# Kernel optimization log

Hardware: AMD Instinct MI355X
Metric: run time of the kernel (lower is better)

## Reference

```python
import jax, jax.numpy as jnp
import numpy as np

POOLED_H = 7
POOLED_W = 7
SPATIAL_SCALE = 0.0625
B, C, H, W = 8, 256, 48, 48
R = 300
IMG = 768  # = H / SPATIAL_SCALE


def setup_inputs() -> dict:
    key = jax.random.key(0)
    k1, k2, k3, k4 = jax.random.split(key, 4)
    features = jax.random.normal(k1, (B, C, H, W), dtype=jnp.float32)
    # rois: (batch_idx, x1, y1, x2, y2) in input-image coords
    bidx = jax.random.randint(k2, (R, 1), 0, B).astype(jnp.float32)
    tl = jax.random.uniform(k3, (R, 2), minval=0.0, maxval=IMG - 64.0)
    wh = jax.random.uniform(k4, (R, 2), minval=32.0, maxval=320.0)
    br = jnp.minimum(tl + wh, IMG - 1.0)
    rois = jnp.concatenate([bidx, tl, br], axis=1).astype(jnp.float32)
    return {"features": features, "rois": rois}


def _hat_integral(x, grid):
    """Integral from -inf to x of the unit hat basis function centered at each
    grid point g (support [g-1, g+1], peak 1, total mass 1).
    x: [..., 1-broadcastable], grid: [G] -> returns [..., G]."""
    t = x[..., None] - (grid - 1.0)
    return jnp.where(
        t <= 0.0, 0.0,
        jnp.where(t <= 1.0, 0.5 * t * t,
                  jnp.where(t <= 2.0, 1.0 - 0.5 * (2.0 - t) ** 2, 1.0)))


def reference(features, rois):
    # Precise RoI Pooling: exact double integral of the bilinear interpolant
    # over each bin, divided by bin area. Bilinear interp (with zero padding
    # outside the map, as in the CUDA PrRoIPoolingGetData) is
    #   f(u,v) = sum_{j,i} feat[j,i] * hat_j(v) * hat_i(u)
    # so the bin integral factorizes into per-axis hat-integral weights.
    Bf, Cf, Hf, Wf = features.shape
    bidx = rois[:, 0].astype(jnp.int32)
    x1 = rois[:, 1] * SPATIAL_SCALE
    y1 = rois[:, 2] * SPATIAL_SCALE
    x2 = rois[:, 3] * SPATIAL_SCALE
    y2 = rois[:, 4] * SPATIAL_SCALE
    roi_w = jnp.maximum(x2 - x1, 0.0)
    roi_h = jnp.maximum(y2 - y1, 0.0)
    bin_w = roi_w / POOLED_W  # [R]
    bin_h = roi_h / POOLED_H

    ph = jnp.arange(POOLED_H, dtype=jnp.float32)
    pw = jnp.arange(POOLED_W, dtype=jnp.float32)
    ya = y1[:, None] + ph[None, :] * bin_h[:, None]  # [R, PH]
    yb = ya + bin_h[:, None]
    xa = x1[:, None] + pw[None, :] * bin_w[:, None]  # [R, PW]
    xb = xa + bin_w[:, None]

    gy = jnp.arange(Hf, dtype=jnp.float32)
    gx = jnp.arange(Wf, dtype=jnp.float32)
    Wy = _hat_integral(yb, gy) - _hat_integral(ya, gy)  # [R, PH, H]
    Wx = _hat_integral(xb, gx) - _hat_integral(xa, gx)  # [R, PW, W]

    feat = features[bidx]  # [R, C, H, W]
    t = jnp.einsum('rpj,rcji->rcpi', Wy, feat)   # integrate over y
    num = jnp.einsum('rqi,rcpi->rcpq', Wx, t)    # integrate over x -> [R,C,PH,PW]

    area = (bin_w * bin_h)[:, None, None, None]  # win_size per ROI
    out = jnp.where(area > 0.0, num / jnp.where(area > 0.0, area, 1.0), 0.0)
    return out
```

## Files before the change

### kernel.cpp

```cpp
#include <hip/hip_runtime.h>


#define PH 7
#define PW 7
#define NBINS 49
#define SCALE 0.0625f
#define CH 256
#define FH 48
#define FW 48
#define RNUM 300
#define CB 8
#define MAXJ 23
#define NL 7

__device__ __forceinline__ float hat_int(float x, float g) {
    float t = x - (g - 1.0f);
    if (t <= 0.0f) return 0.0f;
    if (t <= 1.0f) return 0.5f * t * t;
    if (t <= 2.0f) { float u = 2.0f - t; return 1.0f - 0.5f * u * u; }
    return 1.0f;
}

__global__ __launch_bounds__(256)
void prroi_fused(const float* __restrict__ feat,
                 const float* __restrict__ rois,
                 float* __restrict__ out) {
    const int cblk = blockIdx.x;
    const int r    = blockIdx.y;
    const int c0   = cblk * CB;
    const int tid  = threadIdx.x;

    __shared__ float patch[MAXJ * NL * 32];
    __shared__ float rs[PW * MAXJ * CB];
    __shared__ float pbuf[99];

    const float* roi = rois + r * 5;
    const int   b  = (int)roi[0];
    const float x1 = roi[1] * SCALE, y1 = roi[2] * SCALE;
    const float x2 = roi[3] * SCALE, y2 = roi[4] * SCALE;
    const float ylo = fminf(y1, y2), yhi = fmaxf(y1, y2);
    const float xlo = fminf(x1, x2), xhi = fmaxf(x1, x2);
    const int j1 = min(FH - 1, (int)floorf(yhi) + 1);
    const int i1 = min(FW - 1, (int)floorf(xhi) + 1);
    const int J0 = min(max(0, (int)floorf(ylo) - 1), FH - 6);
    const int I0 = min(max(0, (int)floorf(xlo) - 1) & ~3, FW - 8);
    const int JROWS = min(FH - J0, max(j1 - J0 + 1, 6));
    int NI4 = min(((i1 - I0) >> 2) + 1, (FW - I0) >> 2);
    NI4 = max(NI4, 2);

    const float roi_w = fmaxf(x2 - x1, 0.0f);
    const float bin_w = roi_w / (float)PW;
    const int nA = JROWS * 14;
    int pw1 = 0, q1 = 0, j1r = 0, pw2 = 0, q2 = 0, j2r = 0, bi1 = 0, bi2 = 0;
    float wxa[6], wxb[6];
    const bool a1 = tid < nA, a2 = (tid + 256) < nA;
    if (a1) {
        j1r = tid / 14; const int rem = tid - j1r * 14; pw1 = rem >> 1; q1 = rem & 1;
        const float xa = x1 + pw1 * bin_w, xb = xa + bin_w;
        const int base = min(max((int)floorf(xa) - 1, I0), I0 + 4 * NI4 - 6);
        bi1 = base - I0;
#pragma unroll
        for (int k = 0; k < 6; ++k) {
            const float g = (float)(base + k);
            wxa[k] = hat_int(xb, g) - hat_int(xa, g);
        }
    }
    if (a2) {
        const int v2 = tid + 256;
        j2r = v2 / 14; const int rem = v2 - j2r * 14; pw2 = rem >> 1; q2 = rem & 1;
        const float xa = x1 + pw2 * bin_w, xb = xa + bin_w;
        const int base = min(max((int)floorf(xa) - 1, I0), I0 + 4 * NI4 - 6);
        bi2 = base - I0;
#pragma unroll
        for (int k = 0; k < 6; ++k) {
            const float g = (float)(base + k);
            wxb[k] = hat_int(xb, g) - hat_int(xa, g);
        }
    }

    const float* fb = feat + (size_t)(b * CH + c0) * FH * FW;
    const int J7 = JROWS * NL;
    for (int u = tid; u < 2 * J7; u += 256) {
        const int q  = (u >= J7) ? 1 : 0;
        const int rm = u - q * J7;
        const int j  = rm / NL;
        const int i4 = rm - j * NL;
        if (i4 < NI4) {
            const int ig = I0 + 4 * i4;
            const float* src = fb + ((size_t)(4 * q) * FH + (J0 + j)) * FW + ig;
            const float4 v0  = *(const float4*)(src);
            const float4 v1v = *(const float4*)(src + FH * FW);
            const float4 v2v = *(const float4*)(src + 2 * FH * FW);
            const float4 v3v = *(const float4*)(src + 3 * FH * FW);
            const int msk = (j + i4) & 7;
            float* dl = &patch[(j * NL + i4) * 32];
            *(float4*)(dl + (((0 | q) ^ msk) << 2)) = make_float4(v0.x, v1v.x, v2v.x, v3v.x);
            *(float4*)(dl + (((2 | q) ^ msk) << 2)) = make_float4(v0.y, v1v.y, v2v.y, v3v.y);
            *(float4*)(dl + (((4 | q) ^ msk) << 2)) = make_float4(v0.z, v1v.z, v2v.z, v3v.z);
            *(float4*)(dl + (((6 | q) ^ msk) << 2)) = make_float4(v0.w, v1v.w, v2v.w, v3v.w);
        }
    }

    const float roi_h = fmaxf(y2 - y1, 0.0f);
    const float bin_h = roi_h / (float)PH;
    if (tid < PH) {
        const int ph = tid;
        const float ya = y1 + ph * bin_h, yb = ya + bin_h;
        const int base = min(max((int)floorf(ya) - 1, J0), J0 + JROWS - 6);
        pbuf[84 + ph] = __int_as_float(base - J0);
#pragma unroll
        for (int k = 0; k < 6; ++k) {
            const float g = (float)(base + k);
            pbuf[ph * 6 + k] = hat_int(yb, g) - hat_int(ya, g);
        }
    } else if (tid == PH) {
        const float area = bin_w * bin_h;
        pbuf[98] = (area > 0.0f) ? (1.0f / area) : 0.0f;
    }
    __syncthreads();

    if (a1) {
        float ax = 0.0f, ay = 0.0f, az = 0.0f, aw = 0.0f;
#pragma unroll
        for (int ii = 0; ii < 6; ++ii) {
            const float w = wxa[ii];
            const int i  = bi1 + ii;
            const int i4 = i >> 2, il = i & 3;
            const int slot = ((il << 1) | q1) ^ ((j1r + i4) & 7);
            const float4 v = *(const float4*)(&patch[(j1r * NL + i4) * 32 + (slot << 2)]);
            ax += w * v.x; ay += w * v.y; az += w * v.z; aw += w * v.w;
        }
        *(float4*)(&rs[((size_t)pw1 * MAXJ + j1r) * CB + ((q1 ^ (j1r & 1)) << 2)]) =
            make_float4(ax, ay, az, aw);
    }
    if (a2) {
        float ax = 0.0f, ay = 0.0f, az = 0.0f, aw = 0.0f;
#pragma unroll
        for (int ii = 0; ii < 6; ++ii) {
            const float w = wxb[ii];
            const int i  = bi2 + ii;
            const int i4 = i >> 2, il = i & 3;
            const int slot = ((il << 1) | q2) ^ ((j2r + i4) & 7);
            const float4 v = *(const float4*)(&patch[(j2r * NL + i4) * 32 + (slot << 2)]);
            ax += w * v.x; ay += w * v.y; az += w * v.z; aw += w * v.w;
        }
        *(float4*)(&rs[((size_t)pw2 * MAXJ + j2r) * CB + ((q2 ^ (j2r & 1)) << 2)]) =
            make_float4(ax, ay, az, aw);
    }
    __syncthreads();

    const int bin = tid & 63;
    const int cp  = tid >> 6;
    if (bin < NBINS) {
        const int phv = bin / PW, pwv = bin - phv * PW;
        const int bj = __float_as_int(pbuf[84 + phv]);
        const float inv_area = pbuf[98];
        const int qh = cp >> 1, lo = (cp & 1) * 2;
        float ax = 0.0f, ay = 0.0f;
#pragma unroll
        for (int jj = 0; jj < 6; ++jj) {
            const int j = bj + jj;
            const float w = pbuf[phv * 6 + jj];
            const float2 v = *(const float2*)(
                &rs[((size_t)pwv * MAXJ + j) * CB + ((qh ^ (j & 1)) << 2) + lo]);
            ax += w * v.x; ay += w * v.y;
        }
        float* o = out + ((size_t)r * CH + c0 + 2 * cp) * NBINS + bin;
        o[0]     = ax * inv_area;
        o[NBINS] = ay * inv_area;
    }
}

extern "C" void kernel_launch(void* const* d_in, const int* in_sizes, int n_in,
                              void* d_out, int out_size, void* d_ws, size_t ws_size,
                              hipStream_t stream) {
    const float* feat = (const float*)d_in[0];
    const float* rois = (const float*)d_in[1];
    float* out = (float*)d_out;
    (void)d_ws; (void)ws_size;

    prroi_fused<<<dim3(CH / CB, RNUM), 256, 0, stream>>>(feat, rois, out);
}
```

Baseline: 93.19 us.

## Convert to persistent kernel with register prefetch of next feature patch

Replaces the 9600-block grid with 768 persistent blocks, each handling a contiguous run of 12-13 (ROI, channel-block) work items. While the current item is being reduced from shared memory, the global loads for the next item's feature patch are issued into registers and written to shared memory afterwards. X and Y interpolation weights are recomputed only when the ROI changes. This targets per-block launch and setup cost and hides global-load latency behind compute. In exchange it adds register pressure from the prefetch buffers, an extra barrier when the ROI changes, and a fixed static split of work across blocks.

New measurement: 102.8 us. 1.1x slower.

```diff
diff --git a/kernel.cpp b/kernel.cpp
--- a/kernel.cpp
+++ b/kernel.cpp
@@ -12,6 +12,7 @@
 #define CB 8
 #define MAXJ 23
 #define NL 7
+#define NBLK 768
 
 __device__ __forceinline__ float hat_int(float x, float g) {
     float t = x - (g - 1.0f);
@@ -21,153 +22,217 @@
     return 1.0f;
 }
 
-__global__ __launch_bounds__(256)
-void prroi_fused(const float* __restrict__ feat,
-                 const float* __restrict__ rois,
-                 float* __restrict__ out) {
-    const int cblk = blockIdx.x;
-    const int r    = blockIdx.y;
-    const int c0   = cblk * CB;
+__global__ __launch_bounds__(256, 3)
+void prroi_pers(const float* __restrict__ feat,
+                const float* __restrict__ rois,
+                float* __restrict__ out) {
     const int tid  = threadIdx.x;
+    const int blk  = blockIdx.x;
+    const int base = blk * 12 + min(blk, 384);
+    const int n    = (blk < 384) ? 13 : 12;
 
     __shared__ float patch[MAXJ * NL * 32];
     __shared__ float rs[PW * MAXJ * CB];
     __shared__ float pbuf[99];
 
-    const float* roi = rois + r * 5;
-    const int   b  = (int)roi[0];
-    const float x1 = roi[1] * SCALE, y1 = roi[2] * SCALE;
-    const float x2 = roi[3] * SCALE, y2 = roi[4] * SCALE;
-    const float ylo = fminf(y1, y2), yhi = fmaxf(y1, y2);
-    const float xlo = fminf(x1, x2), xhi = fmaxf(x1, x2);
-    const int j1 = min(FH - 1, (int)floorf(yhi) + 1);
-    const int i1 = min(FW - 1, (int)floorf(xhi) + 1);
-    const int J0 = min(max(0, (int)floorf(ylo) - 1), FH - 6);
-    const int I0 = min(max(0, (int)floorf(xlo) - 1) & ~3, FW - 8);
-    const int JROWS = min(FH - J0, max(j1 - J0 + 1, 6));
-    int NI4 = min(((i1 - I0) >> 2) + 1, (FW - I0) >> 2);
-    NI4 = max(NI4, 2);
-
-    const float roi_w = fmaxf(x2 - x1, 0.0f);
-    const float bin_w = roi_w / (float)PW;
-    const int nA = JROWS * 14;
-    int pw1 = 0, q1 = 0, j1r = 0, pw2 = 0, q2 = 0, j2r = 0, bi1 = 0, bi2 = 0;
+    int rN = 0, c0N = 0, J0N = 0, I0N = 0, JRN = 6, NI4N = 2;
+    float x1N = 0, y1N = 0, x2N = 0, y2N = 0, bwN = 0, bhN = 0, iaN = 0;
+    const float* fbN = feat;
+
+    auto DECODE = [&](int it) {
+        rN  = it >> 5;
+        c0N = (it & 31) << 3;
+        const float* roi = rois + rN * 5;
+        const int b = (int)roi[0];
+        x1N = roi[1] * SCALE; y1N = roi[2] * SCALE;
+        x2N = roi[3] * SCALE; y2N = roi[4] * SCALE;
+        const float ylo = fminf(y1N, y2N), yhi = fmaxf(y1N, y2N);
+        const float xlo = fminf(x1N, x2N), xhi = fmaxf(x1N, x2N);
+        const int j1 = min(FH - 1, (int)floorf(yhi) + 1);
+        const int i1 = min(FW - 1, (int)floorf(xhi) + 1);
+        J0N = min(max(0, (int)floorf(ylo) - 1), FH - 6);
+        I0N = min(max(0, (int)floorf(xlo) - 1) & ~3, FW - 8);
+        JRN = min(FH - J0N, max(j1 - J0N + 1, 6));
+        int ni = min(((i1 - I0N) >> 2) + 1, (FW - I0N) >> 2);
+        NI4N = max(ni, 2);
+        bwN = fmaxf(x2N - x1N, 0.0f) / (float)PW;
+        bhN = fmaxf(y2N - y1N, 0.0f) / (float)PH;
+        const float area = bwN * bhN;
+        iaN = (area > 0.0f) ? (1.0f / area) : 0.0f;
+        fbN = feat + (size_t)(b * CH + c0N) * FH * FW;
+    };
+
+    bool a1 = false, a2 = false;
+    int j1r = 0, pw1 = 0, q1 = 0, bi1 = 0, j2r = 0, pw2 = 0, q2 = 0, bi2 = 0;
     float wxa[6], wxb[6];
-    const bool a1 = tid < nA, a2 = (tid + 256) < nA;
-    if (a1) {
-        j1r = tid / 14; const int rem = tid - j1r * 14; pw1 = rem >> 1; q1 = rem & 1;
-        const float xa = x1 + pw1 * bin_w, xb = xa + bin_w;
-        const int base = min(max((int)floorf(xa) - 1, I0), I0 + 4 * NI4 - 6);
-        bi1 = base - I0;
-#pragma unroll
-        for (int k = 0; k < 6; ++k) {
-            const float g = (float)(base + k);
-            wxa[k] = hat_int(xb, g) - hat_int(xa, g);
-        }
-    }
-    if (a2) {
-        const int v2 = tid + 256;
-        j2r = v2 / 14; const int rem = v2 - j2r * 14; pw2 = rem >> 1; q2 = rem & 1;
-        const float xa = x1 + pw2 * bin_w, xb = xa + bin_w;
-        const int base = min(max((int)floorf(xa) - 1, I0), I0 + 4 * NI4 - 6);
-        bi2 = base - I0;
-#pragma unroll
-        for (int k = 0; k < 6; ++k) {
-            const float g = (float)(base + k);
-            wxb[k] = hat_int(xb, g) - hat_int(xa, g);
-        }
-    }
-
-    const float* fb = feat + (size_t)(b * CH + c0) * FH * FW;
-    const int J7 = JROWS * NL;
-    for (int u = tid; u < 2 * J7; u += 256) {
-        const int q  = (u >= J7) ? 1 : 0;
-        const int rm = u - q * J7;
-        const int j  = rm / NL;
-        const int i4 = rm - j * NL;
-        if (i4 < NI4) {
-            const int ig = I0 + 4 * i4;
-            const float* src = fb + ((size_t)(4 * q) * FH + (J0 + j)) * FW + ig;
-            const float4 v0  = *(const float4*)(src);
-            const float4 v1v = *(const float4*)(src + FH * FW);
-            const float4 v2v = *(const float4*)(src + 2 * FH * FW);
-            const float4 v3v = *(const float4*)(src + 3 * FH * FW);
-            const int msk = (j + i4) & 7;
-            float* dl = &patch[(j * NL + i4) * 32];
-            *(float4*)(dl + (((0 | q) ^ msk) << 2)) = make_float4(v0.x, v1v.x, v2v.x, v3v.x);
-            *(float4*)(dl + (((2 | q) ^ msk) << 2)) = make_float4(v0.y, v1v.y, v2v.y, v3v.y);
-            *(float4*)(dl + (((4 | q) ^ msk) << 2)) = make_float4(v0.z, v1v.z, v2v.z, v3v.z);
-            *(float4*)(dl + (((6 | q) ^ msk) << 2)) = make_float4(v0.w, v1v.w, v2v.w, v3v.w);
-        }
-    }
-
-    const float roi_h = fmaxf(y2 - y1, 0.0f);
-    const float bin_h = roi_h / (float)PH;
-    if (tid < PH) {
-        const int ph = tid;
-        const float ya = y1 + ph * bin_h, yb = ya + bin_h;
-        const int base = min(max((int)floorf(ya) - 1, J0), J0 + JROWS - 6);
-        pbuf[84 + ph] = __int_as_float(base - J0);
-#pragma unroll
-        for (int k = 0; k < 6; ++k) {
-            const float g = (float)(base + k);
-            pbuf[ph * 6 + k] = hat_int(yb, g) - hat_int(ya, g);
-        }
-    } else if (tid == PH) {
-        const float area = bin_w * bin_h;
-        pbuf[98] = (area > 0.0f) ? (1.0f / area) : 0.0f;
-    }
-    __syncthreads();
-
-    if (a1) {
-        float ax = 0.0f, ay = 0.0f, az = 0.0f, aw = 0.0f;
-#pragma unroll
-        for (int ii = 0; ii < 6; ++ii) {
-            const float w = wxa[ii];
-            const int i  = bi1 + ii;
-            const int i4 = i >> 2, il = i & 3;
-            const int slot = ((il << 1) | q1) ^ ((j1r + i4) & 7);
-            const float4 v = *(const float4*)(&patch[(j1r * NL + i4) * 32 + (slot << 2)]);
-            ax += w * v.x; ay += w * v.y; az += w * v.z; aw += w * v.w;
-        }
-        *(float4*)(&rs[((size_t)pw1 * MAXJ + j1r) * CB + ((q1 ^ (j1r & 1)) << 2)]) =
-            make_float4(ax, ay, az, aw);
-    }
-    if (a2) {
-        float ax = 0.0f, ay = 0.0f, az = 0.0f, aw = 0.0f;
-#pragma unroll
-        for (int ii = 0; ii < 6; ++ii) {
-            const float w = wxb[ii];
-            const int i  = bi2 + ii;
-            const int i4 = i >> 2, il = i & 3;
-            const int slot = ((il << 1) | q2) ^ ((j2r + i4) & 7);
-            const float4 v = *(const float4*)(&patch[(j2r * NL + i4) * 32 + (slot << 2)]);
-            ax += w * v.x; ay += w * v.y; az += w * v.z; aw += w * v.w;
-        }
-        *(float4*)(&rs[((size_t)pw2 * MAXJ + j2r) * CB + ((q2 ^ (j2r & 1)) << 2)]) =
-            make_float4(ax, ay, az, aw);
-    }
-    __syncthreads();
-
-    const int bin = tid & 63;
-    const int cp  = tid >> 6;
-    if (bin < NBINS) {
-        const int phv = bin / PW, pwv = bin - phv * PW;
-        const int bj = __float_as_int(pbuf[84 + phv]);
-        const float inv_area = pbuf[98];
-        const int qh = cp >> 1, lo = (cp & 1) * 2;
-        float ax = 0.0f, ay = 0.0f;
-#pragma unroll
-        for (int jj = 0; jj < 6; ++jj) {
-            const int j = bj + jj;
-            const float w = pbuf[phv * 6 + jj];
-            const float2 v = *(const float2*)(
-                &rs[((size_t)pwv * MAXJ + j) * CB + ((qh ^ (j & 1)) << 2) + lo]);
-            ax += w * v.x; ay += w * v.y;
-        }
-        float* o = out + ((size_t)r * CH + c0 + 2 * cp) * NBINS + bin;
-        o[0]     = ax * inv_area;
-        o[NBINS] = ay * inv_area;
+    auto CALC_WX = [&]() {
+        const int nA = JRN * 14;
+        a1 = tid < nA; a2 = (tid + 256) < nA;
+        if (a1) {
+            j1r = tid / 14; const int rem = tid - j1r * 14; pw1 = rem >> 1; q1 = rem & 1;
+            const float xa = x1N + pw1 * bwN, xb = xa + bwN;
+            const int bse = min(max((int)floorf(xa) - 1, I0N), I0N + 4 * NI4N - 6);
+            bi1 = bse - I0N;
+#pragma unroll
+            for (int kk = 0; kk < 6; ++kk) {
+                const float g = (float)(bse + kk);
+                wxa[kk] = hat_int(xb, g) - hat_int(xa, g);
+            }
+        }
+        if (a2) {
+            const int v2 = tid + 256;
+            j2r = v2 / 14; const int rem = v2 - j2r * 14; pw2 = rem >> 1; q2 = rem & 1;
+            const float xa = x1N + pw2 * bwN, xb = xa + bwN;
+            const int bse = min(max((int)floorf(xa) - 1, I0N), I0N + 4 * NI4N - 6);
+            bi2 = bse - I0N;
+#pragma unroll
+            for (int kk = 0; kk < 6; ++kk) {
+                const float g = (float)(bse + kk);
+                wxb[kk] = hat_int(xb, g) - hat_int(xa, g);
+            }
+        }
+    };
+
+    auto CALC_WY = [&]() {
+        if (tid < PH) {
+            const float ya = y1N + tid * bhN, yb = ya + bhN;
+            const int bse = min(max((int)floorf(ya) - 1, J0N), J0N + JRN - 6);
+            pbuf[84 + tid] = __int_as_float(bse - J0N);
+#pragma unroll
+            for (int kk = 0; kk < 6; ++kk) {
+                const float g = (float)(bse + kk);
+                pbuf[tid * 6 + kk] = hat_int(yb, g) - hat_int(ya, g);
+            }
+        } else if (tid == PH) {
+            pbuf[98] = iaN;
+        }
+    };
+
+    float4 pf[2][4];
+    int u_dl[2], u_q[2], u_m[2];
+    bool u_a[2];
+    auto ISSUE = [&]() {
+        const int J7 = JRN * NL;
+#pragma unroll
+        for (int s = 0; s < 2; ++s) {
+            const int v = tid + (s << 8);
+            bool act = v < 2 * J7;
+            if (act) {
+                const int q  = (v >= J7) ? 1 : 0;
+                const int rm = v - (q ? J7 : 0);
+                const int j  = rm / NL;
+                const int i4 = rm - j * NL;
+                act = i4 < NI4N;
+                u_q[s]  = q;
+                u_m[s]  = (j + i4) & 7;
+                u_dl[s] = (j * NL + i4) * 32;
+                if (act) {
+                    const float* src = fbN +
+                        ((size_t)((q << 2) * FH + (J0N + j)) * FW) + I0N + (i4 << 2);
+                    pf[s][0] = *(const float4*)(src);
+                    pf[s][1] = *(const float4*)(src + FH * FW);
+                    pf[s][2] = *(const float4*)(src + 2 * FH * FW);
+                    pf[s][3] = *(const float4*)(src + 3 * FH * FW);
+                }
+            }
+            u_a[s] = act;
+        }
+    };
+
+    auto WRITE_PATCH = [&]() {
+#pragma unroll
+        for (int s = 0; s < 2; ++s) {
+            if (u_a[s]) {
+                float* dl = &patch[u_dl[s]];
+                const int q = u_q[s], m = u_m[s];
+                *(float4*)(dl + (((0 | q) ^ m) << 2)) =
+                    make_float4(pf[s][0].x, pf[s][1].x, pf[s][2].x, pf[s][3].x);
+                *(float4*)(dl + (((2 | q) ^ m) << 2)) =
+                    make_float4(pf[s][0].y, pf[s][1].y, pf[s][2].y, pf[s][3].y);
+                *(float4*)(dl + (((4 | q) ^ m) << 2)) =
+                    make_float4(pf[s][0].z, pf[s][1].z, pf[s][2].z, pf[s][3].z);
+                *(float4*)(dl + (((6 | q) ^ m) << 2)) =
+                    make_float4(pf[s][0].w, pf[s][1].w, pf[s][2].w, pf[s][3].w);
+            }
+        }
+    };
+
+    auto PA = [&]() {
+        if (a1) {
+            float ax = 0.0f, ay = 0.0f, az = 0.0f, aw = 0.0f;
+#pragma unroll
+            for (int ii = 0; ii < 6; ++ii) {
+                const float w = wxa[ii];
+                const int i = bi1 + ii, i4 = i >> 2, il = i & 3;
+                const int slot = ((il << 1) | q1) ^ ((j1r + i4) & 7);
+                const float4 v = *(const float4*)(&patch[(j1r * NL + i4) * 32 + (slot << 2)]);
+                ax += w * v.x; ay += w * v.y; az += w * v.z; aw += w * v.w;
+            }
+            *(float4*)(&rs[((size_t)pw1 * MAXJ + j1r) * CB + ((q1 ^ (j1r & 1)) << 2)]) =
+                make_float4(ax, ay, az, aw);
+        }
+        if (a2) {
+            float ax = 0.0f, ay = 0.0f, az = 0.0f, aw = 0.0f;
+#pragma unroll
+            for (int ii = 0; ii < 6; ++ii) {
+                const float w = wxb[ii];
+                const int i = bi2 + ii, i4 = i >> 2, il = i & 3;
+                const int slot = ((il << 1) | q2) ^ ((j2r + i4) & 7);
+                const float4 v = *(const float4*)(&patch[(j2r * NL + i4) * 32 + (slot << 2)]);
+                ax += w * v.x; ay += w * v.y; az += w * v.z; aw += w * v.w;
+            }
+            *(float4*)(&rs[((size_t)pw2 * MAXJ + j2r) * CB + ((q2 ^ (j2r & 1)) << 2)]) =
+                make_float4(ax, ay, az, aw);
+        }
+    };
+
+    auto PB = [&](int cr, int cc0) {
+        const int bin = tid & 63, cp = tid >> 6;
+        if (bin < NBINS) {
+            const int phv = bin / PW, pwv = bin - phv * PW;
+            const int bj = __float_as_int(pbuf[84 + phv]);
+            const float inv_area = pbuf[98];
+            const int qh = cp >> 1, lo = (cp & 1) * 2;
+            float ax = 0.0f, ay = 0.0f;
+#pragma unroll
+            for (int jj = 0; jj < 6; ++jj) {
+                const int j = bj + jj;
+                const float w = pbuf[phv * 6 + jj];
+                const float2 v = *(const float2*)(
+                    &rs[((size_t)pwv * MAXJ + j) * CB + ((qh ^ (j & 1)) << 2) + lo]);
+                ax += w * v.x; ay += w * v.y;
+            }
+            float* o = out + ((size_t)cr * CH + cc0 + 2 * cp) * NBINS + bin;
+            o[0]     = ax * inv_area;
+            o[NBINS] = ay * inv_area;
+        }
+    };
+
+    DECODE(base);
+    CALC_WX();
+    CALC_WY();
+    ISSUE();
+    WRITE_PATCH();
+    int cur_r = rN, cur_c0 = c0N;
+    if (n > 1) DECODE(base + 1);
+
+    for (int k = 0; k < n; ++k) {
+        __syncthreads();
+        const bool more = (k + 1 < n);
+        if (more) ISSUE();
+        PA();
+        __syncthreads();
+        PB(cur_r, cur_c0);
+        if (more) {
+            WRITE_PATCH();
+            if (rN != cur_r) {
+                __syncthreads();
+                CALC_WX();
+                CALC_WY();
+            }
+            cur_r = rN; cur_c0 = c0N;
+            if (k + 2 < n) DECODE(base + k + 2);
+        }
     }
 }
 
@@ -179,5 +244,5 @@
     float* out = (float*)d_out;
     (void)d_ws; (void)ws_size;
 
-    prroi_fused<<<dim3(CH / CB, RNUM), 256, 0, stream>>>(feat, rois, out);
+    prroi_pers<<<dim3(NBLK), 256, 0, stream>>>(feat, rois, out);
 }
```
